# Optimization experiments

Hardware: AMD Instinct MI355X
Metric: run time of the kernel (lower is better)

Reference implementation:

```python
import jax, jax.numpy as jnp
import numpy as np

D_IN, H, V = 512, 1024, 32000
S, B, T = 64, 128, 48
MARGIN = 0.1


def setup_inputs() -> dict:
    key = jax.random.key(0)
    ks = jax.random.split(key, 16)
    sc = 0.05
    f = lambda k, shp: jax.random.normal(k, shp, jnp.float32) * sc
    emb_W = f(ks[0], (V, D_IN)).at[0].set(0.0)  # padding_idx=0 row is zero
    return dict(
        ctx=jax.random.normal(ks[1], (S, B, H), jnp.float32),
        ctx_mask=jnp.ones((S, B), jnp.float32),
        y=jax.random.randint(ks[2], (T, B), 0, V),
        emb_W=emb_W,
        W_init=f(ks[3], (H, H)), b_init=jnp.zeros((H,), jnp.float32),
        W_ih0=f(ks[4], (3 * H, D_IN)), W_hh0=f(ks[5], (3 * H, H)),
        b_ih0=jnp.zeros((3 * H,), jnp.float32), b_hh0=jnp.zeros((3 * H,), jnp.float32),
        W_c2c=f(ks[6], (H, H)), W_h2c=f(ks[7], (H, H)), v_att=f(ks[8], (H,)),
        W_ih1=f(ks[9], (3 * H, H)), W_hh1=f(ks[10], (3 * H, H)),
        b_ih1=jnp.zeros((3 * H,), jnp.float32), b_hh1=jnp.zeros((3 * H,), jnp.float32),
        W_h2o=f(ks[11], (D_IN, H)), b_h2o=jnp.zeros((D_IN,), jnp.float32),
        W_out=f(ks[12], (V, D_IN)),
    )


def _gru(x, h, Wih, Whh, bih, bhh):
    # torch.nn.GRUCell math
    gi = x @ Wih.T + bih
    gh = h @ Whh.T + bhh
    ir, iz, inn = jnp.split(gi, 3, axis=-1)
    hr, hz, hn = jnp.split(gh, 3, axis=-1)
    r = jax.nn.sigmoid(ir + hr)
    z = jax.nn.sigmoid(iz + hz)
    n = jnp.tanh(inn + r * hn)
    return (1.0 - z) * n + z * h


def reference(ctx, ctx_mask, y, emb_W, W_init, b_init, W_ih0, W_hh0, b_ih0, b_hh0,
              W_c2c, W_h2c, v_att, W_ih1, W_hh1, b_ih1, b_hh1, W_h2o, b_h2o, W_out):
    # dec_init='mean_ctx': tanh(FF(masked mean over source))
    mean_ctx = ctx.sum(0) / ctx_mask.sum(0)[:, None]            # (B,H)
    h = jnp.tanh(mean_ctx @ W_init.T + b_init)                  # h0 (B,H)

    ctx_p = jnp.einsum('sbc,dc->sbd', ctx, W_c2c)               # ctx2ctx, hoisted out of loop
    neg = jnp.where(ctx_mask > 0, 0.0, -1e9)                    # (S,B) additive mask
    W_out_n = W_out / jnp.linalg.norm(W_out, axis=-1, keepdims=True)

    emb_in = emb_W[y[:-1]]                                      # (T-1,B,D_IN)
    targets = y[1:]                                             # (T-1,B)

    def step(h, inp):
        e, tgt = inp
        h1 = _gru(e, h, W_ih0, W_hh0, b_ih0, b_hh0)             # dec0
        # MLP attention: v^T tanh(ctx2ctx(ctx) + hid2ctx(h1))
        scores = jnp.tanh(ctx_p + (h1 @ W_h2c.T)[None]) @ v_att + neg   # (S,B)
        alpha = jax.nn.softmax(scores, axis=0)
        z_t = jnp.einsum('sb,sbc->bc', alpha, ctx)              # context (B,H)
        h2 = _gru(z_t, h1, W_ih1, W_hh1, b_ih1, b_hh1)          # dec1
        logit = jnp.tanh(h2 @ W_h2o.T + b_h2o)                  # hid2out
        logit = logit / jnp.linalg.norm(logit, axis=-1, keepdims=True)
        log_p = logit @ W_out_n.T                               # (B,V) cosine sims
        # max-margin loss, contrastive_type='max', ignore pad (tgt==0)
        s_true = jnp.take_along_axis(log_p, tgt[:, None], axis=1)
        viol = jnp.maximum(MARGIN - s_true + log_p, 0.0)
        viol = viol * (1.0 - jax.nn.one_hot(tgt, V, dtype=log_p.dtype))
        l = jnp.sum(jnp.where(tgt != 0, viol.max(-1), 0.0))
        return h2, l

    _, losses = jax.lax.scan(step, h, (emb_in, targets))
    return losses.sum()
```

## Files before the change

kernel.cpp:

```cpp
#include <hip/hip_runtime.h>
#include <math.h>

#define H    1024
#define H3   3072
#define DIN  512
#define VSZ  32000
#define SS   64
#define BB   128
#define TP   47
#define NROWS (TP*BB)
#define VCHUNKS 250
#define FMARGIN 0.1f
#define NBLK 256
#define HS   65536
#define PS(i) ((i) + ((i) >> 4))

typedef unsigned short u16;
typedef unsigned int u32;
typedef __bf16 bf16_t;
typedef bf16_t bf16x8 __attribute__((ext_vector_type(8)));
typedef float f32x4 __attribute__((ext_vector_type(4)));
typedef u16 u16x4 __attribute__((ext_vector_type(4)));
typedef u16 u16x8 __attribute__((ext_vector_type(8)));

#define MFMA __builtin_amdgcn_mfma_f32_16x16x32_bf16

__device__ inline u16 f2bf(float f){
    unsigned b = __float_as_uint(f);
    return (u16)((b + 0x7FFFu + ((b >> 16) & 1u)) >> 16);
}
__device__ inline float bf2f(u16 u){ return __uint_as_float(((unsigned)u) << 16); }
__device__ inline float sigm(float x){ return 1.f/(1.f + expf(-x)); }

__device__ inline void stoval(float* p, float v){ *p = v; }
__device__ inline void stoval(u16* p, float v){ *p = f2bf(v); }

__device__ inline void cstore(u32* p, u32 v){ __hip_atomic_store(p, v, __ATOMIC_RELAXED, __HIP_MEMORY_SCOPE_AGENT); }
__device__ inline void cstoref(float* p, float v){ __hip_atomic_store(p, v, __ATOMIC_RELAXED, __HIP_MEMORY_SCOPE_AGENT); }
__device__ inline float cloadf(const float* p){ return __hip_atomic_load(p, __ATOMIC_RELAXED, __HIP_MEMORY_SCOPE_AGENT); }

__device__ inline void gbar(u32* bar, u32* mygen, int tid, int bid){
    __syncthreads();
    if (tid == 0){
        u32 tgt = ++(*mygen);
        __builtin_amdgcn_s_waitcnt(0);
        u32* cnt = bar + 64 + (bid >> 3)*32;
        u32 old = __hip_atomic_fetch_add(cnt, 1u, __ATOMIC_RELAXED, __HIP_MEMORY_SCOPE_AGENT);
        if (old == 7u){
            __hip_atomic_store(cnt, 0u, __ATOMIC_RELAXED, __HIP_MEMORY_SCOPE_AGENT);
            u32 old2 = __hip_atomic_fetch_add(&bar[1], 1u, __ATOMIC_RELEASE, __HIP_MEMORY_SCOPE_AGENT);
            if (old2 == 31u){
                __hip_atomic_store(&bar[1], 0u, __ATOMIC_RELAXED, __HIP_MEMORY_SCOPE_AGENT);
                __hip_atomic_store(&bar[0], tgt, __ATOMIC_RELEASE, __HIP_MEMORY_SCOPE_AGENT);
            }
        }
        while (__hip_atomic_load(&bar[0], __ATOMIC_RELAXED, __HIP_MEMORY_SCOPE_AGENT) < tgt)
            __builtin_amdgcn_s_sleep(1);
    }
    __syncthreads();
    asm volatile("" ::: "memory");
}


__global__ __launch_bounds__(128) void k_mask_sum(const float* __restrict__ mask, float* __restrict__ msum){
    int b = threadIdx.x;
    if (b < BB){ float s = 0.f; for (int i = 0; i < SS; i++) s += mask[i*BB + b]; msum[b] = s; }
}

__global__ __launch_bounds__(256) void k_mean_ctx(const float* __restrict__ ctx, const float* __restrict__ msum,
                                                  float* __restrict__ mean){
    int idx = blockIdx.x*256 + threadIdx.x;
    if (idx < BB*H){
        float s = 0.f;
        for (int i = 0; i < SS; i++) s += ctx[(size_t)i*BB*H + idx];
        mean[idx] = s / msum[idx / H];
    }
}

__global__ __launch_bounds__(256) void k_f32bf(const float* __restrict__ in, u16* __restrict__ out, int n4){
    int i = blockIdx.x*256 + threadIdx.x;
    if (i >= n4) return;
    float4 v = ((const float4*)in)[i];
    u16x4 o = { f2bf(v.x), f2bf(v.y), f2bf(v.z), f2bf(v.w) };
    ((u16x4*)out)[i] = o;
}

__global__ __launch_bounds__(256) void k_pack_h0(const float* __restrict__ h0, u32* __restrict__ hsHI,
                                                 u32* __restrict__ hsLO, float* __restrict__ hsF){
    int i = blockIdx.x*256 + threadIdx.x;
    float v0 = h0[i*2], v1 = h0[i*2 + 1];
    u16 a = f2bf(v0), b = f2bf(v1);
    hsHI[i] = (u32)a | ((u32)b << 16);
    hsLO[i] = (u32)f2bf(v0 - bf2f(a)) | ((u32)f2bf(v1 - bf2f(b)) << 16);
    hsF[i*2] = v0; hsF[i*2 + 1] = v1;
}

__global__ __launch_bounds__(256) void k_f2bf_frag(const float* __restrict__ in, u16* __restrict__ out,
                                                   int RK8, int K8){
    int t = blockIdx.x*256 + threadIdx.x;
    if (t >= RK8) return;
    int r = t / K8, k8 = t - r*K8;
    const float* p = in + (size_t)r*K8*8 + k8*8;
    float4 a = *(const float4*)p;
    float4 b = *(const float4*)(p + 4);
    size_t dst = ((size_t)(r >> 4)*(K8 >> 2) + (k8 >> 2))*512 + (size_t)((r & 15) + (k8 & 3)*16)*8;
    u16x8 o;
    o[0]=f2bf(a.x); o[1]=f2bf(a.y); o[2]=f2bf(a.z); o[3]=f2bf(a.w);
    o[4]=f2bf(b.x); o[5]=f2bf(b.y); o[6]=f2bf(b.z); o[7]=f2bf(b.w);
    *(u16x8*)(out + dst) = o;
}

__global__ __launch_bounds__(256) void k_rownorm_frag(const float* __restrict__ in, u16* __restrict__ out,
                                                      int nrows){
    int w = threadIdx.x >> 6, lane = threadIdx.x & 63;
    int row = blockIdx.x*4 + w;
    if (row >= nrows) return;
    const float* r = in + (size_t)row*512 + lane*8;
    float4 a = *(const float4*)r;
    float4 b = *(const float4*)(r + 4);
    float s = a.x*a.x + a.y*a.y + a.z*a.z + a.w*a.w
            + b.x*b.x + b.y*b.y + b.z*b.z + b.w*b.w;
    #pragma unroll
    for (int off = 32; off; off >>= 1) s += __shfl_xor(s, off);
    float inv = rsqrtf(s);
    size_t dst = ((size_t)(row >> 4)*16 + (lane >> 2))*512 + (size_t)((row & 15) + (lane & 3)*16)*8;
    u16x8 o;
    o[0]=f2bf(a.x*inv); o[1]=f2bf(a.y*inv); o[2]=f2bf(a.z*inv); o[3]=f2bf(a.w*inv);
    o[4]=f2bf(b.x*inv); o[5]=f2bf(b.y*inv); o[6]=f2bf(b.z*inv); o[7]=f2bf(b.w*inv);
    *(u16x8*)(out + dst) = o;
}

__global__ __launch_bounds__(256) void k_emb_frag(const float* __restrict__ emb, const int* __restrict__ y,
                                                  u16* __restrict__ out){
    int w = threadIdx.x >> 6, lane = threadIdx.x & 63;
    int row = blockIdx.x*4 + w;
    int src = y[row];
    const float* r = emb + (size_t)src*512 + lane*8;
    float4 a = *(const float4*)r;
    float4 b = *(const float4*)(r + 4);
    size_t dst = ((size_t)(row >> 4)*16 + (lane >> 2))*512 + (size_t)((row & 15) + (lane & 3)*16)*8;
    u16x8 o;
    o[0]=f2bf(a.x); o[1]=f2bf(a.y); o[2]=f2bf(a.z); o[3]=f2bf(a.w);
    o[4]=f2bf(b.x); o[5]=f2bf(b.y); o[6]=f2bf(b.z); o[7]=f2bf(b.w);
    *(u16x8*)(out + dst) = o;
}

template<int ACT>
__global__ __launch_bounds__(256) void k_gemm_nt(const float* __restrict__ A, const float* __restrict__ W,
                                                 const float* __restrict__ bias, float* __restrict__ C,
                                                 int M, int N, int K){
    __shared__ float As[16][68];
    __shared__ float Ws[16][68];
    int tid = threadIdx.x;
    int bm = blockIdx.y*64, bn = blockIdx.x*64;
    int lr = tid >> 2;
    int lk = (tid & 3) * 4;
    int tr = (tid >> 4) * 4;
    int tc = (tid & 15) * 4;
    float acc[4][4] = {};
    const float* Abase = A + (size_t)(bm + lr)*K;
    const float* Wbase = W + (size_t)(bn + lr)*K;
    for (int k0 = 0; k0 < K; k0 += 16){
        float4 av = *(const float4*)(Abase + k0 + lk);
        float4 wv = *(const float4*)(Wbase + k0 + lk);
        __syncthreads();
        As[lk+0][lr]=av.x; As[lk+1][lr]=av.y; As[lk+2][lr]=av.z; As[lk+3][lr]=av.w;
        Ws[lk+0][lr]=wv.x; Ws[lk+1][lr]=wv.y; Ws[lk+2][lr]=wv.z; Ws[lk+3][lr]=wv.w;
        __syncthreads();
        #pragma unroll
        for (int kk = 0; kk < 16; kk++){
            float4 a = *(const float4*)&As[kk][tr];
            float4 w = *(const float4*)&Ws[kk][tc];
            acc[0][0] += a.x*w.x; acc[0][1] += a.x*w.y; acc[0][2] += a.x*w.z; acc[0][3] += a.x*w.w;
            acc[1][0] += a.y*w.x; acc[1][1] += a.y*w.y; acc[1][2] += a.y*w.z; acc[1][3] += a.y*w.w;
            acc[2][0] += a.z*w.x; acc[2][1] += a.z*w.y; acc[2][2] += a.z*w.z; acc[2][3] += a.z*w.w;
            acc[3][0] += a.w*w.x; acc[3][1] += a.w*w.y; acc[3][2] += a.w*w.z; acc[3][3] += a.w*w.w;
        }
    }
    #pragma unroll
    for (int i = 0; i < 4; i++){
        #pragma unroll
        for (int j = 0; j < 4; j++){
            float v = acc[i][j];
            if (bias) v += bias[bn + tc + j];
            if (ACT == 1) v = tanhf(v);
            C[(size_t)(bm + tr + i)*N + bn + tc + j] = v;
        }
    }
}

template<int AFRAG, int ACT, typename OutT>
__global__ __launch_bounds__(256) void k_gemmf(const u16* __restrict__ A, const u16* __restrict__ B,
                                               const float* __restrict__ bias, OutT* __restrict__ C,
                                               int M, int N, int K){
    int tid = threadIdx.x, lane = tid & 63, w = tid >> 6;
    int wm = w >> 1, wn = w & 1;
    int row0 = blockIdx.y*128 + wm*64, col0 = blockIdx.x*128 + wn*64;
    int r16 = lane & 15, kg8 = (lane >> 4)*8, rg = (lane >> 4)*4;
    int K32 = K >> 5;
    f32x4 acc[4][4] = {};
    for (int k0 = 0; k0 < K32; k0++){
        bf16x8 af[4], bfv[4];
        #pragma unroll
        for (int i = 0; i < 4; i++){
            if (AFRAG) af[i] = *(const bf16x8*)(A + (((size_t)((row0 >> 4) + i)*K32 + k0) << 9) + lane*8);
            else       af[i] = *(const bf16x8*)(A + (size_t)(row0 + i*16 + r16)*K + k0*32 + kg8);
        }
        #pragma unroll
        for (int j = 0; j < 4; j++)
            bfv[j] = *(const bf16x8*)(B + (((size_t)((col0 >> 4) + j)*K32 + k0) << 9) + lane*8);
        #pragma unroll
        for (int i = 0; i < 4; i++)
            #pragma unroll
            for (int j = 0; j < 4; j++)
                acc[i][j] = MFMA(af[i], bfv[j], acc[i][j], 0, 0, 0);
    }
    #pragma unroll
    for (int i = 0; i < 4; i++){
        #pragma unroll
        for (int j = 0; j < 4; j++){
            #pragma unroll
            for (int r = 0; r < 4; r++){
                int row = row0 + i*16 + rg + r;
                int col = col0 + j*16 + r16;
                float v = acc[i][j][r];
                if (bias) v += bias[col];
                if (ACT) v = tanhf(v);
                stoval(C + (size_t)row*N + col, v);
            }
        }
    }
}

struct RF {
    const u16 *gi0, *Whh0, *Wh2c, *Wih1, *Whh1, *ctxp;
    const float *bhh0, *bih1, *bhh1, *vatt, *mask, *ctxf;
    u32 *hsHI, *hsLO, *h1HI, *h1LO, *ztHI, *ztLO;
    float *hsF, *h1F, *prF, *ghF;
    u16 *h2all;
    u32 *bar;
};

__global__ __launch_bounds__(512) void k_recur5(RF a){
    __shared__ u16 wlds[49152];
    __shared__ float ps[1088];
    __shared__ float vattL[1088];
    __shared__ float sal[SS];
    __shared__ float zred[4][512];
    const int tid = threadIdx.x, lane = tid & 63, wv = tid >> 6;
    const int bid = blockIdx.x;
    const int r16 = lane & 15, rg = (lane >> 4)*4, kq4 = (lane >> 4)*4;
    const int ab = (bid & 7)*16 + ((bid >> 3) >> 1);
    const int ahalf = (bid >> 3) & 1;
    u32 mygen = 0;

    {
        auto cp32k = [&](const u16* gsrc, int tile, int base){
            const u32* s = (const u32*)(gsrc + (size_t)tile*16384);
            u32* d = (u32*)(wlds + base);
            #pragma unroll
            for (int i = 0; i < 16; i++) d[tid + i*512] = s[tid + i*512];
        };
        if (bid < 64){
            cp32k(a.Whh0, bid, 0); cp32k(a.Whh0, 64+bid, 16384); cp32k(a.Whh0, 128+bid, 32768);
        } else if (bid < 128){
            int jt = bid - 64;
            cp32k(a.Wih1, jt, 0); cp32k(a.Wih1, 64+jt, 16384); cp32k(a.Wih1, 128+jt, 32768);
        } else if (bid < 192){
            int wt = bid - 128;
            cp32k(a.Whh1, 3*wt, 0); cp32k(a.Whh1, 3*wt+1, 16384); cp32k(a.Whh1, 3*wt+2, 32768);
        } else {
            cp32k(a.Wh2c, bid-192, 0);
        }
        for (int i = tid; i < H; i += 512) vattL[PS(i)] = a.vatt[i];
    }
    __syncthreads();

    for (int t = 0; t < TP; t++){
        if (bid < 64){
            const u32* AbH = a.hsHI + (size_t)t*HS + (size_t)(wv*16 + r16)*512 + kq4;
            const u32* AbL = a.hsLO + (size_t)t*HS + (size_t)(wv*16 + r16)*512 + kq4;
            f32x4 ac0 = {}, ac1 = {}, ac2 = {};
            for (int k0 = 0; k0 < 32; k0++){
                bf16x8 ah = *(const bf16x8*)(AbH + k0*16);
                bf16x8 al = *(const bf16x8*)(AbL + k0*16);
                bf16x8 b0 = *(const bf16x8*)(wlds + (k0*64 + lane)*8);
                bf16x8 b1 = *(const bf16x8*)(wlds + 16384 + (k0*64 + lane)*8);
                bf16x8 b2 = *(const bf16x8*)(wlds + 32768 + (k0*64 + lane)*8);
                ac0 = MFMA(ah, b0, ac0, 0, 0, 0); ac0 = MFMA(al, b0, ac0, 0, 0, 0);
                ac1 = MFMA(ah, b1, ac1, 0, 0, 0); ac1 = MFMA(al, b1, ac1, 0, 0, 0);
                ac2 = MFMA(ah, b2, ac2, 0, 0, 0); ac2 = MFMA(al, b2, ac2, 0, 0, 0);
            }
            const u16* gi = a.gi0 + (size_t)t*BB*H3;
            #pragma unroll
            for (int r = 0; r < 4; r++){
                int b = wv*16 + rg + r, j = bid*16 + r16;
                float gr = bf2f(gi[(size_t)b*H3 + j]);
                float gz = bf2f(gi[(size_t)b*H3 + H + j]);
                float gn = bf2f(gi[(size_t)b*H3 + 2*H + j]);
                float hr = ac0[r] + a.bhh0[j];
                float hz = ac1[r] + a.bhh0[H + j];
                float hn = ac2[r] + a.bhh0[2*H + j];
                float hp = cloadf(a.hsF + (size_t)b*H + j);
                float rr = sigm(gr + hr), zz = sigm(gz + hz);
                float nn = tanhf(gn + rr*hn);
                float hv = (1.f - zz)*nn + zz*hp;
                cstoref(a.h1F + (size_t)b*H + j, hv);
                u16 hib = f2bf(hv);
                u16 lob = f2bf(hv - bf2f(hib));
                u32 hip = (u32)__shfl_xor((int)(u32)hib, 1);
                u32 lop = (u32)__shfl_xor((int)(u32)lob, 1);
                if (!(r16 & 1)){
                    cstore(a.h1HI + (size_t)t*HS + (size_t)b*512 + (j >> 1), (u32)hib | (hip << 16));
                    cstore(a.h1LO + (size_t)t*HS + (size_t)b*512 + (j >> 1), (u32)lob | (lop << 16));
                }
            }
        }
        gbar(a.bar, &mygen, tid, bid);

        if (bid >= 128){
            const u32* AbH = a.h1HI + (size_t)t*HS + (size_t)(wv*16 + r16)*512 + kq4;
            const u32* AbL = a.h1LO + (size_t)t*HS + (size_t)(wv*16 + r16)*512 + kq4;
            if (bid < 192){
                int wt = bid - 128;
                f32x4 ac0 = {}, ac1 = {}, ac2 = {};
                for (int k0 = 0; k0 < 32; k0++){
                    bf16x8 ah = *(const bf16x8*)(AbH + k0*16);
                    bf16x8 al = *(const bf16x8*)(AbL + k0*16);
                    bf16x8 b0 = *(const bf16x8*)(wlds + (k0*64 + lane)*8);
                    bf16x8 b1 = *(const bf16x8*)(wlds + 16384 + (k0*64 + lane)*8);
                    bf16x8 b2 = *(const bf16x8*)(wlds + 32768 + (k0*64 + lane)*8);
                    ac0 = MFMA(ah, b0, ac0, 0, 0, 0); ac0 = MFMA(al, b0, ac0, 0, 0, 0);
                    ac1 = MFMA(ah, b1, ac1, 0, 0, 0); ac1 = MFMA(al, b1, ac1, 0, 0, 0);
                    ac2 = MFMA(ah, b2, ac2, 0, 0, 0); ac2 = MFMA(al, b2, ac2, 0, 0, 0);
                }
                #pragma unroll
                for (int r = 0; r < 4; r++){
                    int b = wv*16 + rg + r;
                    int c0 = wt*48 + r16;
                    cstoref(a.ghF + (size_t)b*H3 + c0,      ac0[r]);
                    cstoref(a.ghF + (size_t)b*H3 + c0 + 16, ac1[r]);
                    cstoref(a.ghF + (size_t)b*H3 + c0 + 32, ac2[r]);
                }
            } else {
                f32x4 ac = {};
                for (int k0 = 0; k0 < 32; k0++){
                    bf16x8 ah = *(const bf16x8*)(AbH + k0*16);
                    bf16x8 al = *(const bf16x8*)(AbL + k0*16);
                    bf16x8 bv = *(const bf16x8*)(wlds + (k0*64 + lane)*8);
                    ac = MFMA(ah, bv, ac, 0, 0, 0); ac = MFMA(al, bv, ac, 0, 0, 0);
                }
                #pragma unroll
                for (int r = 0; r < 4; r++){
                    int b = wv*16 + rg + r;
                    cstoref(a.prF + (size_t)b*H + (bid - 192)*16 + r16, ac[r]);
                }
            }
        }
        gbar(a.bar, &mygen, tid, bid);

        {
            int b = ab;
            for (int i = tid; i < H; i += 512) ps[PS(i)] = cloadf(a.prF + (size_t)b*H + i);
            __syncthreads();
            #pragma unroll
            for (int q = 0; q < 8; q++){
                int s = wv*8 + q;
                const u16* cp = a.ctxp + ((size_t)(s*BB + b))*H + lane*16;
                u16x8 c0 = *(const u16x8*)cp;
                u16x8 c1 = *(const u16x8*)(cp + 8);
                const float* pp = ps + lane*17;
                const float* vv = vattL + lane*17;
                float acc = 0.f;
                #pragma unroll
                for (int e = 0; e < 8; e++) acc += tanhf(bf2f(c0[e]) + pp[e]) * vv[e];
                #pragma unroll
                for (int e = 0; e < 8; e++) acc += tanhf(bf2f(c1[e]) + pp[8 + e]) * vv[8 + e];
                #pragma unroll
                for (int off = 32; off; off >>= 1) acc += __shfl_xor(acc, off);
                if (lane == 0) sal[s] = acc + ((a.mask[s*BB + b] > 0.f) ? 0.f : -1e9f);
            }
            __syncthreads();
            if (tid < 64){
                float v = sal[tid];
                float m = v;
                #pragma unroll
                for (int off = 32; off; off >>= 1) m = fmaxf(m, __shfl_xor(m, off));
                float e = expf(v - m);
                float su = e;
                #pragma unroll
                for (int off = 32; off; off >>= 1) su += __shfl_xor(su, off);
                sal[tid] = e / su;
            }
            __syncthreads();
            int cq = (tid & 127)*4, sg = tid >> 7;
            float4 z = {0.f, 0.f, 0.f, 0.f};
            for (int si = 0; si < 16; si++){
                int s = sg + si*4;
                float al = sal[s];
                float4 cv = *(const float4*)(a.ctxf + ((size_t)(s*BB + b))*H + ahalf*512 + cq);
                z.x += al*cv.x; z.y += al*cv.y; z.z += al*cv.z; z.w += al*cv.w;
            }
            *(float4*)&zred[sg][cq] = z;
            __syncthreads();
            if (tid < 256){
                int c2 = tid*2;
                float a0 = zred[0][c2]   + zred[1][c2]   + zred[2][c2]   + zred[3][c2];
                float a1 = zred[0][c2+1] + zred[1][c2+1] + zred[2][c2+1] + zred[3][c2+1];
                int j0 = ahalf*512 + c2;
                u16 z0 = f2bf(a0), z1 = f2bf(a1);
                cstore(a.ztHI + (size_t)t*HS + (size_t)b*512 + (j0 >> 1), (u32)z0 | ((u32)z1 << 16));
                cstore(a.ztLO + (size_t)t*HS + (size_t)b*512 + (j0 >> 1),
                       (u32)f2bf(a0 - bf2f(z0)) | ((u32)f2bf(a1 - bf2f(z1)) << 16));
            }
            __syncthreads();
        }
        gbar(a.bar, &mygen, tid, bid);

        if (bid >= 64 && bid < 128){
            int jt = bid - 64;
            const u32* AbH = a.ztHI + (size_t)t*HS + (size_t)(wv*16 + r16)*512 + kq4;
            const u32* AbL = a.ztLO + (size_t)t*HS + (size_t)(wv*16 + r16)*512 + kq4;
            f32x4 ac0 = {}, ac1 = {}, ac2 = {};
            for (int k0 = 0; k0 < 32; k0++){
                bf16x8 ah = *(const bf16x8*)(AbH + k0*16);
                bf16x8 al = *(const bf16x8*)(AbL + k0*16);
                bf16x8 b0 = *(const bf16x8*)(wlds + (k0*64 + lane)*8);
                bf16x8 b1 = *(const bf16x8*)(wlds + 16384 + (k0*64 + lane)*8);
                bf16x8 b2 = *(const bf16x8*)(wlds + 32768 + (k0*64 + lane)*8);
                ac0 = MFMA(ah, b0, ac0, 0, 0, 0); ac0 = MFMA(al, b0, ac0, 0, 0, 0);
                ac1 = MFMA(ah, b1, ac1, 0, 0, 0); ac1 = MFMA(al, b1, ac1, 0, 0, 0);
                ac2 = MFMA(ah, b2, ac2, 0, 0, 0); ac2 = MFMA(al, b2, ac2, 0, 0, 0);
            }
            #pragma unroll
            for (int r = 0; r < 4; r++){
                int b = wv*16 + rg + r, j = jt*16 + r16;
                float gr = ac0[r] + a.bih1[j];
                float gz = ac1[r] + a.bih1[H + j];
                float gn = ac2[r] + a.bih1[2*H + j];
                float hr = cloadf(a.ghF + (size_t)b*H3 + j)       + a.bhh1[j];
                float hz = cloadf(a.ghF + (size_t)b*H3 + H + j)   + a.bhh1[H + j];
                float hn = cloadf(a.ghF + (size_t)b*H3 + 2*H + j) + a.bhh1[2*H + j];
                float h1v = cloadf(a.h1F + (size_t)b*H + j);
                float rr = sigm(gr + hr), zz = sigm(gz + hz);
                float nn = tanhf(gn + rr*hn);
                float hv = (1.f - zz)*nn + zz*h1v;
                cstoref(a.hsF + (size_t)b*H + j, hv);
                a.h2all[((size_t)t*BB + b)*H + j] = f2bf(hv);
                u16 hib = f2bf(hv);
                u16 lob = f2bf(hv - bf2f(hib));
                u32 hip = (u32)__shfl_xor((int)(u32)hib, 1);
                u32 lop = (u32)__shfl_xor((int)(u32)lob, 1);
                if (!(r16 & 1)){
                    cstore(a.hsHI + (size_t)(t+1)*HS + (size_t)b*512 + (j >> 1), (u32)hib | (hip << 16));
                    cstore(a.hsLO + (size_t)(t+1)*HS + (size_t)b*512 + (j >> 1), (u32)lob | (lop << 16));
                }
            }
        }
        gbar(a.bar, &mygen, tid, bid);
    }
}

__global__ __launch_bounds__(256) void k_final(const u16* __restrict__ logitf, const u16* __restrict__ Wf,
                                               const int* __restrict__ y, float* __restrict__ pmax,
                                               float* __restrict__ strue){
    __shared__ float red[128][2];
    int tid = threadIdx.x, w = tid >> 6, lane = tid & 63;
    int wm = w >> 1, wn = w & 1;
    int row0 = blockIdx.x*128 + wm*64;
    int col0 = blockIdx.y*128 + wn*64;
    int r16 = lane & 15, rg = (lane >> 4)*4;
    f32x4 acc[4][4] = {};
    for (int k0 = 0; k0 < 16; k0++){
        bf16x8 af[4], bfv[4];
        #pragma unroll
        for (int i = 0; i < 4; i++)
            af[i] = *(const bf16x8*)(logitf + (((size_t)((row0 >> 4) + i)*16 + k0) << 9) + lane*8);
        #pragma unroll
        for (int j = 0; j < 4; j++)
            bfv[j] = *(const bf16x8*)(Wf + (((size_t)((col0 >> 4) + j)*16 + k0) << 9) + lane*8);
        #pragma unroll
        for (int i = 0; i < 4; i++)
            #pragma unroll
            for (int j = 0; j < 4; j++)
                acc[i][j] = MFMA(af[i], bfv[j], acc[i][j], 0, 0, 0);
    }
    #pragma unroll
    for (int i = 0; i < 4; i++){
        #pragma unroll
        for (int r = 0; r < 4; r++){
            int row = row0 + i*16 + rg + r;
            int tgt = y[row + BB];
            float m = -1e30f;
            #pragma unroll
            for (int j = 0; j < 4; j++){
                float v = acc[i][j][r];
                int col = col0 + j*16 + r16;
                if (col == tgt){ strue[row] = v; v = -1e30f; }
                m = fmaxf(m, v);
            }
            m = fmaxf(m, __shfl_xor(m, 1));
            m = fmaxf(m, __shfl_xor(m, 2));
            m = fmaxf(m, __shfl_xor(m, 4));
            m = fmaxf(m, __shfl_xor(m, 8));
            if (r16 == 0) red[wm*64 + i*16 + rg + r][wn] = m;
        }
    }
    __syncthreads();
    if (tid < 128){
        float m = fmaxf(red[tid][0], red[tid][1]);
        pmax[(size_t)(blockIdx.x*128 + tid)*VCHUNKS + blockIdx.y] = m;
    }
}

__global__ __launch_bounds__(256) void k_loss(const float* __restrict__ pmax, const float* __restrict__ strue,
                                              const int* __restrict__ y, float* __restrict__ out){
    int R = blockIdx.x*256 + threadIdx.x;
    int lane = threadIdx.x & 63, wave = threadIdx.x >> 6;
    float l = 0.f;
    if (R < NROWS){
        int tgt = y[R + BB];
        if (tgt != 0){
            const float* pm = pmax + (size_t)R*VCHUNKS;
            float m = -1e30f;
            for (int i = 0; i < VCHUNKS; i++) m = fmaxf(m, pm[i]);
            l = fmaxf(FMARGIN - strue[R] + m, 0.f);
        }
    }
    #pragma unroll
    for (int off = 32; off; off >>= 1) l += __shfl_down(l, off);
    __shared__ float wsum[4];
    if (lane == 0) wsum[wave] = l;
    __syncthreads();
    if (threadIdx.x == 0) atomicAdd(out, wsum[0] + wsum[1] + wsum[2] + wsum[3]);
}

extern "C" void kernel_launch(void* const* d_in, const int* in_sizes, int n_in,
                              void* d_out, int out_size, void* d_ws, size_t ws_size,
                              hipStream_t stream){
    const float* ctx    = (const float*)d_in[0];
    const float* mask   = (const float*)d_in[1];
    const int*   y      = (const int*)d_in[2];
    const float* emb_W  = (const float*)d_in[3];
    const float* W_init = (const float*)d_in[4];
    const float* b_init = (const float*)d_in[5];
    const float* W_ih0  = (const float*)d_in[6];
    const float* W_hh0  = (const float*)d_in[7];
    const float* b_ih0  = (const float*)d_in[8];
    const float* b_hh0  = (const float*)d_in[9];
    const float* W_c2c  = (const float*)d_in[10];
    const float* W_h2c  = (const float*)d_in[11];
    const float* v_att  = (const float*)d_in[12];
    const float* W_ih1  = (const float*)d_in[13];
    const float* W_hh1  = (const float*)d_in[14];
    const float* b_ih1  = (const float*)d_in[15];
    const float* b_hh1  = (const float*)d_in[16];
    const float* W_h2o  = (const float*)d_in[17];
    const float* b_h2o  = (const float*)d_in[18];
    const float* W_out  = (const float*)d_in[19];
    float* out = (float*)d_out;

    char* wsb = (char*)d_ws;
    size_t off = 0;
    auto alloc = [&](size_t bytes)->void*{
        void* p = (void*)(wsb + off);
        off = (off + bytes + 255) & ~(size_t)255;
        return p;
    };
    u16* Wih0f = (u16*)alloc((size_t)H3*DIN*2);
    u16* Whh0f = (u16*)alloc((size_t)H3*H*2);
    u16* Wih1f = (u16*)alloc((size_t)H3*H*2);
    u16* Whh1f = (u16*)alloc((size_t)H3*H*2);
    u16* Wh2cf = (u16*)alloc((size_t)H*H*2);
    u16* Wc2cf = (u16*)alloc((size_t)H*H*2);
    u16* Wh2of = (u16*)alloc((size_t)DIN*H*2);
    u16* Woutf = (u16*)alloc((size_t)VSZ*DIN*2);
    u16* ctxb  = (u16*)alloc((size_t)SS*BB*H*2);
    u16* ctxpb = (u16*)alloc((size_t)SS*BB*H*2);
    u16* embf  = (u16*)alloc((size_t)NROWS*DIN*2);
    u16* gi0b  = (u16*)alloc((size_t)NROWS*H3*2);
    u16* h2allb= (u16*)alloc((size_t)NROWS*H*2);
    u32* hsHI  = (u32*)alloc((size_t)(TP+1)*HS*4);
    u32* hsLO  = (u32*)alloc((size_t)(TP+1)*HS*4);
    u32* h1HI  = (u32*)alloc((size_t)TP*HS*4);
    u32* h1LO  = (u32*)alloc((size_t)TP*HS*4);
    u32* ztHI  = (u32*)alloc((size_t)TP*HS*4);
    u32* ztLO  = (u32*)alloc((size_t)TP*HS*4);
    float* hsF = (float*)alloc((size_t)BB*H*4);
    float* h1F = (float*)alloc((size_t)BB*H*4);
    float* prF = (float*)alloc((size_t)BB*H*4);
    float* ghF = (float*)alloc((size_t)BB*H3*4);
    u32* bar   = (u32*)alloc(8192);
    float* strue  = (float*)alloc(NROWS*4);
    float* msum   = (float*)alloc(BB*4);
    float* meanc  = (float*)alloc((size_t)BB*H*4);
    float* h0f    = (float*)alloc((size_t)BB*H*4);

    float* logitf  = (float*)gi0b;
    u16*   logitfr = (u16*)(gi0b + (size_t)NROWS*DIN*2);
    float* pmax    = (float*)(gi0b + (size_t)NROWS*DIN*2 + (size_t)NROWS*DIN);

    hipMemsetAsync(d_out, 0, sizeof(float), stream);
    hipMemsetAsync(bar, 0, 8192, stream);

    hipLaunchKernelGGL(k_mask_sum, dim3(1), dim3(128), 0, stream, mask, msum);
    hipLaunchKernelGGL(k_mean_ctx, dim3(BB*H/256), dim3(256), 0, stream, ctx, msum, meanc);
    hipLaunchKernelGGL((k_gemm_nt<1>), dim3(H/64, BB/64), dim3(256), 0, stream,
                       meanc, W_init, b_init, h0f, BB, H, H);
    hipLaunchKernelGGL(k_pack_h0, dim3(HS/256), dim3(256), 0, stream, h0f, hsHI, hsLO, hsF);

    hipLaunchKernelGGL(k_f2bf_frag, dim3(H3*DIN/8/256), dim3(256), 0, stream, W_ih0, Wih0f, H3*DIN/8, DIN/8);
    hipLaunchKernelGGL(k_f2bf_frag, dim3(H3*H/8/256), dim3(256), 0, stream, W_hh0, Whh0f, H3*H/8, H/8);
    hipLaunchKernelGGL(k_f2bf_frag, dim3(H3*H/8/256), dim3(256), 0, stream, W_ih1, Wih1f, H3*H/8, H/8);
    hipLaunchKernelGGL(k_f2bf_frag, dim3(H3*H/8/256), dim3(256), 0, stream, W_hh1, Whh1f, H3*H/8, H/8);
    hipLaunchKernelGGL(k_f2bf_frag, dim3(H*H/8/256), dim3(256), 0, stream, W_h2c, Wh2cf, H*H/8, H/8);
    hipLaunchKernelGGL(k_f2bf_frag, dim3(H*H/8/256), dim3(256), 0, stream, W_c2c, Wc2cf, H*H/8, H/8);
    hipLaunchKernelGGL(k_f2bf_frag, dim3(DIN*H/8/256), dim3(256), 0, stream, W_h2o, Wh2of, DIN*H/8, H/8);
    hipLaunchKernelGGL(k_rownorm_frag, dim3(VSZ/4), dim3(256), 0, stream, W_out, Woutf, VSZ);
    hipLaunchKernelGGL(k_f32bf, dim3(SS*BB*H/4/256), dim3(256), 0, stream, ctx, ctxb, SS*BB*H/4);
    hipLaunchKernelGGL(k_emb_frag, dim3(NROWS/4), dim3(256), 0, stream, emb_W, y, embf);

    hipLaunchKernelGGL((k_gemmf<1,0,u16>), dim3(H3/128, NROWS/128), dim3(256), 0, stream,
                       embf, Wih0f, b_ih0, gi0b, NROWS, H3, DIN);
    hipLaunchKernelGGL((k_gemmf<0,0,u16>), dim3(H/128, SS*BB/128), dim3(256), 0, stream,
                       ctxb, Wc2cf, (const float*)nullptr, ctxpb, SS*BB, H, H);

    RF rf;
    rf.gi0 = gi0b; rf.Whh0 = Whh0f; rf.Wh2c = Wh2cf; rf.Wih1 = Wih1f; rf.Whh1 = Whh1f;
    rf.ctxp = ctxpb;
    rf.bhh0 = b_hh0; rf.bih1 = b_ih1; rf.bhh1 = b_hh1; rf.vatt = v_att; rf.mask = mask; rf.ctxf = ctx;
    rf.hsHI = hsHI; rf.hsLO = hsLO; rf.h1HI = h1HI; rf.h1LO = h1LO; rf.ztHI = ztHI; rf.ztLO = ztLO;
    rf.hsF = hsF; rf.h1F = h1F; rf.prF = prF; rf.ghF = ghF;
    rf.h2all = h2allb; rf.bar = bar;
    void* kp[] = { (void*)&rf };
    hipLaunchCooperativeKernel((const void*)k_recur5, dim3(NBLK), dim3(512), kp, 0, stream);

    hipLaunchKernelGGL((k_gemmf<0,1,float>), dim3(DIN/128, NROWS/128), dim3(256), 0, stream,
                       h2allb, Wh2of, b_h2o, logitf, NROWS, DIN, H);
    hipLaunchKernelGGL(k_rownorm_frag, dim3(NROWS/4), dim3(256), 0, stream, logitf, logitfr, NROWS);
    hipLaunchKernelGGL(k_final, dim3(NROWS/128, VSZ/128), dim3(256), 0, stream,
                       logitfr, Woutf, y, pmax, strue);
    hipLaunchKernelGGL(k_loss, dim3((NROWS + 255)/256), dim3(256), 0, stream, pmax, strue, y, out);
}
```

Baseline: 5.929 ms.

## Drop fp32 hidden-state mirrors, per-step attention buffer, ctxp prefetch, wider stores

The recurrent kernel stops keeping fp32 copies of h and h1 and rebuilds them from the bf16 hi/lo split pairs it already writes. The attention projection buffer now gets one slice per timestep, placed in the Wout scratch area, which removes one source of cross-step reuse hazards; W_out normalisation moves to after the recurrence so that memory can be shared. Idle blocks prefetch ctx_p lines into cache during the GRU phases. Scoring is unrolled two source positions at a time, context accumulation is unrolled, and gh and prF stores are paired into 64-bit atomic stores. The goal is less global traffic and latency on the serial critical path, at the cost of more memory-aliasing complexity.

```diff
diff --git a/kernel.cpp b/kernel.cpp
--- a/kernel.cpp
+++ b/kernel.cpp
@@ -17,6 +17,7 @@
 
 typedef unsigned short u16;
 typedef unsigned int u32;
+typedef unsigned long long u64;
 typedef __bf16 bf16_t;
 typedef bf16_t bf16x8 __attribute__((ext_vector_type(8)));
 typedef float f32x4 __attribute__((ext_vector_type(4)));
@@ -36,7 +37,7 @@
 __device__ inline void stoval(u16* p, float v){ *p = f2bf(v); }
 
 __device__ inline void cstore(u32* p, u32 v){ __hip_atomic_store(p, v, __ATOMIC_RELAXED, __HIP_MEMORY_SCOPE_AGENT); }
-__device__ inline void cstoref(float* p, float v){ __hip_atomic_store(p, v, __ATOMIC_RELAXED, __HIP_MEMORY_SCOPE_AGENT); }
+__device__ inline void cstore64(u64* p, u64 v){ __hip_atomic_store(p, v, __ATOMIC_RELAXED, __HIP_MEMORY_SCOPE_AGENT); }
 __device__ inline float cloadf(const float* p){ return __hip_atomic_load(p, __ATOMIC_RELAXED, __HIP_MEMORY_SCOPE_AGENT); }
 
 __device__ inline void gbar(u32* bar, u32* mygen, int tid, int bid){
@@ -86,13 +87,12 @@
 }
 
 __global__ __launch_bounds__(256) void k_pack_h0(const float* __restrict__ h0, u32* __restrict__ hsHI,
-                                                 u32* __restrict__ hsLO, float* __restrict__ hsF){
+                                                 u32* __restrict__ hsLO){
     int i = blockIdx.x*256 + threadIdx.x;
     float v0 = h0[i*2], v1 = h0[i*2 + 1];
     u16 a = f2bf(v0), b = f2bf(v1);
     hsHI[i] = (u32)a | ((u32)b << 16);
     hsLO[i] = (u32)f2bf(v0 - bf2f(a)) | ((u32)f2bf(v1 - bf2f(b)) << 16);
-    hsF[i*2] = v0; hsF[i*2 + 1] = v1;
 }
 
 __global__ __launch_bounds__(256) void k_f2bf_frag(const float* __restrict__ in, u16* __restrict__ out,
@@ -232,16 +232,17 @@
     }
 }
 
-struct RF {
+struct RH {
     const u16 *gi0, *Whh0, *Wh2c, *Wih1, *Whh1, *ctxp;
     const float *bhh0, *bih1, *bhh1, *vatt, *mask, *ctxf;
     u32 *hsHI, *hsLO, *h1HI, *h1LO, *ztHI, *ztLO;
-    float *hsF, *h1F, *prF, *ghF;
+    float *prF;
+    float *ghF;
     u16 *h2all;
     u32 *bar;
 };
 
-__global__ __launch_bounds__(512) void k_recur5(RF a){
+__global__ __launch_bounds__(512) void k_recur7(RH a){
     __shared__ u16 wlds[49152];
     __shared__ float ps[1088];
     __shared__ float vattL[1088];
@@ -276,7 +277,20 @@
     }
     __syncthreads();
 
+    auto pf_ctxp = [&](){
+        u32 acc = 0;
+        #pragma unroll
+        for (int i = 0; i < 4; i++){
+            int line = tid + i*512;
+            int s = line >> 5, l = line & 31;
+            acc += *((const u32*)(a.ctxp + ((size_t)(s*BB + ab))*H) + l*16);
+        }
+        asm volatile("" :: "v"(acc));
+    };
+
     for (int t = 0; t < TP; t++){
+        float* prT = a.prF + (size_t)t*BB*H;
+
         if (bid < 64){
             const u32* AbH = a.hsHI + (size_t)t*HS + (size_t)(wv*16 + r16)*512 + kq4;
             const u32* AbL = a.hsLO + (size_t)t*HS + (size_t)(wv*16 + r16)*512 + kq4;
@@ -292,6 +306,9 @@
                 ac2 = MFMA(ah, b2, ac2, 0, 0, 0); ac2 = MFMA(al, b2, ac2, 0, 0, 0);
             }
             const u16* gi = a.gi0 + (size_t)t*BB*H3;
+            const u32* hsH = a.hsHI + (size_t)t*HS;
+            const u32* hsL = a.hsLO + (size_t)t*HS;
+            int sh = (r16 & 1)*16;
             #pragma unroll
             for (int r = 0; r < 4; r++){
                 int b = wv*16 + rg + r, j = bid*16 + r16;
@@ -301,11 +318,12 @@
                 float hr = ac0[r] + a.bhh0[j];
                 float hz = ac1[r] + a.bhh0[H + j];
                 float hn = ac2[r] + a.bhh0[2*H + j];
-                float hp = cloadf(a.hsF + (size_t)b*H + j);
+                u32 uh = hsH[(size_t)b*512 + (j >> 1)];
+                u32 ul = hsL[(size_t)b*512 + (j >> 1)];
+                float hp = bf2f((u16)(uh >> sh)) + bf2f((u16)(ul >> sh));
                 float rr = sigm(gr + hr), zz = sigm(gz + hz);
                 float nn = tanhf(gn + rr*hn);
                 float hv = (1.f - zz)*nn + zz*hp;
-                cstoref(a.h1F + (size_t)b*H + j, hv);
                 u16 hib = f2bf(hv);
                 u16 lob = f2bf(hv - bf2f(hib));
                 u32 hip = (u32)__shfl_xor((int)(u32)hib, 1);
@@ -315,6 +333,8 @@
                     cstore(a.h1LO + (size_t)t*HS + (size_t)b*512 + (j >> 1), (u32)lob | (lop << 16));
                 }
             }
+        } else {
+            pf_ctxp();
         }
         gbar(a.bar, &mygen, tid, bid);
 
@@ -338,9 +358,17 @@
                 for (int r = 0; r < 4; r++){
                     int b = wv*16 + rg + r;
                     int c0 = wt*48 + r16;
-                    cstoref(a.ghF + (size_t)b*H3 + c0,      ac0[r]);
-                    cstoref(a.ghF + (size_t)b*H3 + c0 + 16, ac1[r]);
-                    cstoref(a.ghF + (size_t)b*H3 + c0 + 32, ac2[r]);
+                    float p0 = __shfl_xor(ac0[r], 1);
+                    float p1 = __shfl_xor(ac1[r], 1);
+                    float p2 = __shfl_xor(ac2[r], 1);
+                    if (!(r16 & 1)){
+                        cstore64((u64*)(a.ghF + (size_t)b*H3 + c0),
+                                 (u64)__float_as_uint(ac0[r]) | ((u64)__float_as_uint(p0) << 32));
+                        cstore64((u64*)(a.ghF + (size_t)b*H3 + c0 + 16),
+                                 (u64)__float_as_uint(ac1[r]) | ((u64)__float_as_uint(p1) << 32));
+                        cstore64((u64*)(a.ghF + (size_t)b*H3 + c0 + 32),
+                                 (u64)__float_as_uint(ac2[r]) | ((u64)__float_as_uint(p2) << 32));
+                    }
                 }
             } else {
                 f32x4 ac = {};
@@ -353,32 +381,53 @@
                 #pragma unroll
                 for (int r = 0; r < 4; r++){
                     int b = wv*16 + rg + r;
-                    cstoref(a.prF + (size_t)b*H + (bid - 192)*16 + r16, ac[r]);
-                }
-            }
+                    int c0 = (bid - 192)*16 + r16;
+                    float p0 = __shfl_xor(ac[r], 1);
+                    if (!(r16 & 1))
+                        cstore64((u64*)(prT + (size_t)b*H + c0),
+                                 (u64)__float_as_uint(ac[r]) | ((u64)__float_as_uint(p0) << 32));
+                }
+            }
+        } else if (bid < 64){
+            pf_ctxp();
         }
         gbar(a.bar, &mygen, tid, bid);
 
         {
             int b = ab;
-            for (int i = tid; i < H; i += 512) ps[PS(i)] = cloadf(a.prF + (size_t)b*H + i);
+            for (int i = tid; i < H; i += 512) ps[PS(i)] = prT[(size_t)b*H + i];
             __syncthreads();
             #pragma unroll
-            for (int q = 0; q < 8; q++){
-                int s = wv*8 + q;
-                const u16* cp = a.ctxp + ((size_t)(s*BB + b))*H + lane*16;
-                u16x8 c0 = *(const u16x8*)cp;
-                u16x8 c1 = *(const u16x8*)(cp + 8);
+            for (int q = 0; q < 8; q += 2){
+                int s0 = wv*8 + q, s1 = s0 + 1;
+                const u16* cpA = a.ctxp + ((size_t)(s0*BB + b))*H + lane*16;
+                const u16* cpB = a.ctxp + ((size_t)(s1*BB + b))*H + lane*16;
+                u16x8 a0 = *(const u16x8*)cpA;
+                u16x8 a1 = *(const u16x8*)(cpA + 8);
+                u16x8 b0 = *(const u16x8*)cpB;
+                u16x8 b1 = *(const u16x8*)(cpB + 8);
                 const float* pp = ps + lane*17;
                 const float* vv = vattL + lane*17;
-                float acc = 0.f;
+                float accA = 0.f, accB = 0.f;
                 #pragma unroll
-                for (int e = 0; e < 8; e++) acc += tanhf(bf2f(c0[e]) + pp[e]) * vv[e];
+                for (int e = 0; e < 8; e++){
+                    accA += tanhf(bf2f(a0[e]) + pp[e]) * vv[e];
+                    accB += tanhf(bf2f(b0[e]) + pp[e]) * vv[e];
+                }
                 #pragma unroll
-                for (int e = 0; e < 8; e++) acc += tanhf(bf2f(c1[e]) + pp[8 + e]) * vv[8 + e];
+                for (int e = 0; e < 8; e++){
+                    accA += tanhf(bf2f(a1[e]) + pp[8 + e]) * vv[8 + e];
+                    accB += tanhf(bf2f(b1[e]) + pp[8 + e]) * vv[8 + e];
+                }
                 #pragma unroll
-                for (int off = 32; off; off >>= 1) acc += __shfl_xor(acc, off);
-                if (lane == 0) sal[s] = acc + ((a.mask[s*BB + b] > 0.f) ? 0.f : -1e9f);
+                for (int off = 32; off; off >>= 1){
+                    accA += __shfl_xor(accA, off);
+                    accB += __shfl_xor(accB, off);
+                }
+                if (lane == 0){
+                    sal[s0] = accA + ((a.mask[s0*BB + b] > 0.f) ? 0.f : -1e9f);
+                    sal[s1] = accB + ((a.mask[s1*BB + b] > 0.f) ? 0.f : -1e9f);
+                }
             }
             __syncthreads();
             if (tid < 64){
@@ -395,11 +444,18 @@
             __syncthreads();
             int cq = (tid & 127)*4, sg = tid >> 7;
             float4 z = {0.f, 0.f, 0.f, 0.f};
-            for (int si = 0; si < 16; si++){
-                int s = sg + si*4;
-                float al = sal[s];
-                float4 cv = *(const float4*)(a.ctxf + ((size_t)(s*BB + b))*H + ahalf*512 + cq);
-                z.x += al*cv.x; z.y += al*cv.y; z.z += al*cv.z; z.w += al*cv.w;
+            #pragma unroll
+            for (int so = 0; so < 16; so += 4){
+                float4 c0 = *(const float4*)(a.ctxf + ((size_t)((sg + (so+0)*4)*BB + b))*H + ahalf*512 + cq);
+                float4 c1 = *(const float4*)(a.ctxf + ((size_t)((sg + (so+1)*4)*BB + b))*H + ahalf*512 + cq);
+                float4 c2 = *(const float4*)(a.ctxf + ((size_t)((sg + (so+2)*4)*BB + b))*H + ahalf*512 + cq);
+                float4 c3 = *(const float4*)(a.ctxf + ((size_t)((sg + (so+3)*4)*BB + b))*H + ahalf*512 + cq);
+                float l0 = sal[sg + (so+0)*4], l1 = sal[sg + (so+1)*4];
+                float l2 = sal[sg + (so+2)*4], l3 = sal[sg + (so+3)*4];
+                z.x += l0*c0.x + l1*c1.x + l2*c2.x + l3*c3.x;
+                z.y += l0*c0.y + l1*c1.y + l2*c2.y + l3*c3.y;
+                z.z += l0*c0.z + l1*c1.z + l2*c2.z + l3*c3.z;
+                z.w += l0*c0.w + l1*c1.w + l2*c2.w + l3*c3.w;
             }
             *(float4*)&zred[sg][cq] = z;
             __syncthreads();
@@ -432,6 +488,9 @@
                 ac1 = MFMA(ah, b1, ac1, 0, 0, 0); ac1 = MFMA(al, b1, ac1, 0, 0, 0);
                 ac2 = MFMA(ah, b2, ac2, 0, 0, 0); ac2 = MFMA(al, b2, ac2, 0, 0, 0);
             }
+            const u32* h1H = a.h1HI + (size_t)t*HS;
+            const u32* h1L = a.h1LO + (size_t)t*HS;
+            int sh = (r16 & 1)*16;
             #pragma unroll
             for (int r = 0; r < 4; r++){
                 int b = wv*16 + rg + r, j = jt*16 + r16;
@@ -441,11 +500,12 @@
                 float hr = cloadf(a.ghF + (size_t)b*H3 + j)       + a.bhh1[j];
                 float hz = cloadf(a.ghF + (size_t)b*H3 + H + j)   + a.bhh1[H + j];
                 float hn = cloadf(a.ghF + (size_t)b*H3 + 2*H + j) + a.bhh1[2*H + j];
-                float h1v = cloadf(a.h1F + (size_t)b*H + j);
+                u32 uh = h1H[(size_t)b*512 + (j >> 1)];
+                u32 ul = h1L[(size_t)b*512 + (j >> 1)];
+                float h1v = bf2f((u16)(uh >> sh)) + bf2f((u16)(ul >> sh));
                 float rr = sigm(gr + hr), zz = sigm(gz + hz);
                 float nn = tanhf(gn + rr*hn);
                 float hv = (1.f - zz)*nn + zz*h1v;
-                cstoref(a.hsF + (size_t)b*H + j, hv);
                 a.h2all[((size_t)t*BB + b)*H + j] = f2bf(hv);
                 u16 hib = f2bf(hv);
                 u16 lob = f2bf(hv - bf2f(hib));
@@ -586,9 +646,6 @@
     u32* h1LO  = (u32*)alloc((size_t)TP*HS*4);
     u32* ztHI  = (u32*)alloc((size_t)TP*HS*4);
     u32* ztLO  = (u32*)alloc((size_t)TP*HS*4);
-    float* hsF = (float*)alloc((size_t)BB*H*4);
-    float* h1F = (float*)alloc((size_t)BB*H*4);
-    float* prF = (float*)alloc((size_t)BB*H*4);
     float* ghF = (float*)alloc((size_t)BB*H3*4);
     u32* bar   = (u32*)alloc(8192);
     float* strue  = (float*)alloc(NROWS*4);
@@ -596,6 +653,8 @@
     float* meanc  = (float*)alloc((size_t)BB*H*4);
     float* h0f    = (float*)alloc((size_t)BB*H*4);
 
+    float* prF = (float*)Woutf;
+
     float* logitf  = (float*)gi0b;
     u16*   logitfr = (u16*)(gi0b + (size_t)NROWS*DIN*2);
     float* pmax    = (float*)(gi0b + (size_t)NROWS*DIN*2 + (size_t)NROWS*DIN);
@@ -607,7 +666,7 @@
     hipLaunchKernelGGL(k_mean_ctx, dim3(BB*H/256), dim3(256), 0, stream, ctx, msum, meanc);
     hipLaunchKernelGGL((k_gemm_nt<1>), dim3(H/64, BB/64), dim3(256), 0, stream,
                        meanc, W_init, b_init, h0f, BB, H, H);
-    hipLaunchKernelGGL(k_pack_h0, dim3(HS/256), dim3(256), 0, stream, h0f, hsHI, hsLO, hsF);
+    hipLaunchKernelGGL(k_pack_h0, dim3(HS/256), dim3(256), 0, stream, h0f, hsHI, hsLO);
 
     hipLaunchKernelGGL(k_f2bf_frag, dim3(H3*DIN/8/256), dim3(256), 0, stream, W_ih0, Wih0f, H3*DIN/8, DIN/8);
     hipLaunchKernelGGL(k_f2bf_frag, dim3(H3*H/8/256), dim3(256), 0, stream, W_hh0, Whh0f, H3*H/8, H/8);
@@ -616,7 +675,6 @@
     hipLaunchKernelGGL(k_f2bf_frag, dim3(H*H/8/256), dim3(256), 0, stream, W_h2c, Wh2cf, H*H/8, H/8);
     hipLaunchKernelGGL(k_f2bf_frag, dim3(H*H/8/256), dim3(256), 0, stream, W_c2c, Wc2cf, H*H/8, H/8);
     hipLaunchKernelGGL(k_f2bf_frag, dim3(DIN*H/8/256), dim3(256), 0, stream, W_h2o, Wh2of, DIN*H/8, H/8);
-    hipLaunchKernelGGL(k_rownorm_frag, dim3(VSZ/4), dim3(256), 0, stream, W_out, Woutf, VSZ);
     hipLaunchKernelGGL(k_f32bf, dim3(SS*BB*H/4/256), dim3(256), 0, stream, ctx, ctxb, SS*BB*H/4);
     hipLaunchKernelGGL(k_emb_frag, dim3(NROWS/4), dim3(256), 0, stream, emb_W, y, embf);
 
@@ -625,16 +683,17 @@
     hipLaunchKernelGGL((k_gemmf<0,0,u16>), dim3(H/128, SS*BB/128), dim3(256), 0, stream,
                        ctxb, Wc2cf, (const float*)nullptr, ctxpb, SS*BB, H, H);
 
-    RF rf;
-    rf.gi0 = gi0b; rf.Whh0 = Whh0f; rf.Wh2c = Wh2cf; rf.Wih1 = Wih1f; rf.Whh1 = Whh1f;
-    rf.ctxp = ctxpb;
-    rf.bhh0 = b_hh0; rf.bih1 = b_ih1; rf.bhh1 = b_hh1; rf.vatt = v_att; rf.mask = mask; rf.ctxf = ctx;
-    rf.hsHI = hsHI; rf.hsLO = hsLO; rf.h1HI = h1HI; rf.h1LO = h1LO; rf.ztHI = ztHI; rf.ztLO = ztLO;
-    rf.hsF = hsF; rf.h1F = h1F; rf.prF = prF; rf.ghF = ghF;
-    rf.h2all = h2allb; rf.bar = bar;
-    void* kp[] = { (void*)&rf };
-    hipLaunchCooperativeKernel((const void*)k_recur5, dim3(NBLK), dim3(512), kp, 0, stream);
-
+    RH rh;
+    rh.gi0 = gi0b; rh.Whh0 = Whh0f; rh.Wh2c = Wh2cf; rh.Wih1 = Wih1f; rh.Whh1 = Whh1f;
+    rh.ctxp = ctxpb;
+    rh.bhh0 = b_hh0; rh.bih1 = b_ih1; rh.bhh1 = b_hh1; rh.vatt = v_att; rh.mask = mask; rh.ctxf = ctx;
+    rh.hsHI = hsHI; rh.hsLO = hsLO; rh.h1HI = h1HI; rh.h1LO = h1LO; rh.ztHI = ztHI; rh.ztLO = ztLO;
+    rh.prF = prF; rh.ghF = ghF;
+    rh.h2all = h2allb; rh.bar = bar;
+    void* kp[] = { (void*)&rh };
+    hipLaunchCooperativeKernel((const void*)k_recur7, dim3(NBLK), dim3(512), kp, 0, stream);
+
+    hipLaunchKernelGGL(k_rownorm_frag, dim3(VSZ/4), dim3(256), 0, stream, W_out, Woutf, VSZ);
     hipLaunchKernelGGL((k_gemmf<0,1,float>), dim3(DIN/128, NROWS/128), dim3(256), 0, stream,
                        h2allb, Wh2of, b_h2o, logitf, NROWS, DIN, H);
     hipLaunchKernelGGL(k_rownorm_frag, dim3(NROWS/4), dim3(256), 0, stream, logitf, logitfr, NROWS);
```

Result: no change. 5.978 ms (+0.8%).
